# Optimization experiments

Measured on AMD Instinct MI355X. Metric: run time of the kernel, lower is better.

Reference implementation:

```python
import jax, jax.numpy as jnp
import numpy as np

DIM, H, DH = 3072, 24, 128
MLP = int(DIM * 4.0)
EPS = 1e-6


def setup_inputs() -> dict:
    key = jax.random.key(0)
    ks = jax.random.split(key, 8)
    B, L = 2, 4096
    s = 0.02
    return {
        "hidden_states": jax.random.normal(ks[0], (B, L, DIM), jnp.float32),
        "temb": jax.random.normal(ks[1], (B, DIM), jnp.float32),
        "rope": jax.random.normal(ks[2], (L, DH // 2, 4), jnp.float32),
        "w_lin": jax.random.normal(ks[3], (DIM, 3 * DIM), jnp.float32) * s,
        "b_lin": jnp.zeros((3 * DIM,), jnp.float32),
        "w1": jax.random.normal(ks[4], (DIM, 3 * DIM + MLP), jnp.float32) * s,
        "b1": jnp.zeros((3 * DIM + MLP,), jnp.float32),
        "w2": jax.random.normal(ks[5], (DIM + MLP, DIM), jnp.float32) * s,
        "b2": jnp.zeros((DIM,), jnp.float32),
        "q_scale": jnp.ones((DH,), jnp.float32),
        "k_scale": jnp.ones((DH,), jnp.float32),
    }


def _rms(x, scale):
    return x * jax.lax.rsqrt(jnp.mean(x * x, axis=-1, keepdims=True) + EPS) * scale


def _rope(x, fr):
    # x: [B,H,L,DH]; fr: [L, DH//2, 2, 2]
    B, Hn, L, D = x.shape
    x_ = x.reshape(B, Hn, L, D // 2, 1, 2)
    out = fr[..., 0] * x_[..., 0] + fr[..., 1] * x_[..., 1]  # [B,H,L,D//2,2]
    return out.reshape(B, Hn, L, D)


def reference(hidden_states, temb, rope, w_lin, b_lin, w1, b1, w2, b2, q_scale, k_scale):
    B, L, _ = hidden_states.shape
    residual = hidden_states
    # AdaLayerNormZeroSingle
    emb = jax.nn.silu(temb) @ w_lin + b_lin  # [B, 3*DIM]
    shift, scale, gate = jnp.split(emb[:, None, :], 3, axis=-1)
    mu = jnp.mean(hidden_states, axis=-1, keepdims=True)
    var = jnp.mean(jnp.square(hidden_states - mu), axis=-1, keepdims=True)
    x = (hidden_states - mu) * jax.lax.rsqrt(var + EPS)
    x = x * (1 + scale) + shift
    # fused QKV + MLP projection
    proj = x @ w1 + b1
    qkv, mlp = proj[..., : 3 * DIM], proj[..., 3 * DIM :]
    qkv = qkv.reshape(B, L, 3, H, DH).transpose(2, 0, 3, 1, 4)  # [3,B,H,L,DH]
    q, k, v = qkv[0], qkv[1], qkv[2]
    q = _rms(q, q_scale)
    k = _rms(k, k_scale)
    fr = rope.reshape(L, DH // 2, 2, 2)
    q = _rope(q, fr)
    k = _rope(k, fr)
    # heads are MERGED before attention (faithful to source)
    q = q.transpose(0, 2, 1, 3).reshape(B, L, H * DH)
    k = k.transpose(0, 2, 1, 3).reshape(B, L, H * DH)
    v = v.transpose(0, 2, 1, 3).reshape(B, L, H * DH)
    attn = jax.nn.softmax(jnp.einsum("bqd,bkd->bqk", q, k) * (DH ** -0.5), axis=-1)
    attn_out = jnp.einsum("bqk,bkd->bqd", attn, v)
    h = jnp.concatenate([attn_out, jax.nn.gelu(mlp)], axis=-1) @ w2 + b2
    return residual + gate * h
```

## Files before the change

kernel.cpp:

```cpp
#include <hip/hip_runtime.h>
#include <hip/hip_fp16.h>

typedef _Float16 half_t;
typedef __attribute__((ext_vector_type(8))) _Float16 f16x8;
typedef __attribute__((ext_vector_type(4))) float f32x4;

#define DIM   3072
#define NH    24
#define DH    128
#define MLP_D 12288
#define LSEQ  4096
#define BATCH 2
#define NROWS 8192
#define N1    21504
#define QKV_N 9216
#define CAT_N 15360

__device__ __forceinline__ void gload16(const void* g, void* l) {
  __builtin_amdgcn_global_load_lds((const __attribute__((address_space(1))) void*)g,
                                   (__attribute__((address_space(3))) void*)l, 16, 0, 0);
}

__device__ __forceinline__ float gelu_tanh(float x) {
  float u = 0.7978845608028654f * (x + 0.044715f * x * x * x);
  float t = 1.f - 2.f / (__expf(2.f * u) + 1.f);
  return 0.5f * x * (1.f + t);
}

struct EpiParams {
  const float* bias;
  float* outF; int ldoF;
  half_t* o1; int ldo1;
  half_t* o2; int ldo2;
  const float* resid;
  const float* gate;
  float scale;
};

template<int EPI>
__global__ __launch_bounds__(512, 2) void gemm256(
    const half_t* __restrict__ A, int lda,
    const half_t* __restrict__ B, int ldb,
    int nbx, int nby, int nsplit, int K, EpiParams ep)
{
  __shared__ __align__(16) char lds[131072];
  const int t = threadIdx.x, lane = t & 63, wid = t >> 6;

  const int nwg = nbx * nby;
  const int wg = blockIdx.x;
  const int id = (wg & 7) * (nwg >> 3) + (wg >> 3);
  const int panel = 8 * nbx;
  const int bm = (id / panel) * 8 + (id % 8);
  const int bn = (id % panel) / 8;
  const int brow = bm * 256, bcol = bn * 256;
  const int wr = wid >> 2, wc = wid & 3;

  f32x4 acc[8][4];
#pragma unroll
  for (int m = 0; m < 8; ++m)
#pragma unroll
    for (int n = 0; n < 4; ++n) acc[m][n] = (f32x4){0.f, 0.f, 0.f, 0.f};

  const int scol = (((lane & 3) ^ ((lane >> 3) & 3)) * 8);
  const half_t* pA = A + (size_t)(brow + wid * 32 + (lane >> 2)) * lda + scol;
  const half_t* pB = B + (size_t)(bcol + wid * 32 + (lane >> 2)) * ldb + scol;
  const int wrow = wid * 2048;
  const int NT = K >> 5;

  const int pc = (((lane >> 4) ^ ((lane >> 1) & 3)) << 4);
  const int arow = (wr * 128 + (lane & 15)) * 64 + pc;
  const int brow_o = 16384 + (wc * 64 + (lane & 15)) * 64 + pc;

  f16x8 af[4], af2[4], bfA[4], bfB[4];

#define STAGE(tk) {                                                         \
    char* sb = lds + (((tk) & 3) << 15);                                    \
    const half_t* ga = pA + (size_t)(tk) * 32;                              \
    const half_t* gb = pB + (size_t)(tk) * 32;                              \
    gload16(ga, sb + wrow);                                                 \
    gload16(ga + (size_t)16 * lda, sb + wrow + 1024);                       \
    gload16(gb, sb + 16384 + wrow);                                         \
    gload16(gb + (size_t)16 * ldb, sb + 16384 + wrow + 1024); }

#define MFMAC(base, AF, BF)                                                 \
    __builtin_amdgcn_s_setprio(1);                                          \
    _Pragma("unroll")                                                       \
    for (int mi = 0; mi < 4; ++mi)                                          \
      _Pragma("unroll")                                                     \
      for (int nj = 0; nj < 4; ++nj)                                        \
        acc[(base) + mi][nj] = __builtin_amdgcn_mfma_f32_16x16x32_f16(      \
            AF[mi], BF[nj], acc[(base) + mi][nj], 0, 0, 0);                 \
    __builtin_amdgcn_s_setprio(0);

#define BODY(tt, BFC, BFN) {                                                \
    char* cb = lds + (((tt) & 3) << 15);                                    \
    af2[0] = *(const f16x8*)(cb + arow + 4096);                             \
    af2[1] = *(const f16x8*)(cb + arow + 5120);                             \
    af2[2] = *(const f16x8*)(cb + arow + 6144);                             \
    af2[3] = *(const f16x8*)(cb + arow + 7168);                             \
    MFMAC(0, af, BFC)                                                       \
    if ((tt) + 3 < NT) STAGE((tt) + 3);                                     \
    __builtin_amdgcn_sched_barrier(0);                                      \
    if ((tt) + 3 < NT)      asm volatile("s_waitcnt vmcnt(8)" ::: "memory");\
    else if ((tt) + 2 < NT) asm volatile("s_waitcnt vmcnt(4)" ::: "memory");\
    else                    asm volatile("s_waitcnt vmcnt(0)" ::: "memory");\
    __builtin_amdgcn_s_barrier();                                           \
    __builtin_amdgcn_sched_barrier(0);                                      \
    if ((tt) + 1 < NT) {                                                    \
      char* fb = lds + ((((tt) + 1) & 3) << 15);                            \
      af[0] = *(const f16x8*)(fb + arow);                                   \
      af[1] = *(const f16x8*)(fb + arow + 1024);                            \
      af[2] = *(const f16x8*)(fb + arow + 2048);                            \
      af[3] = *(const f16x8*)(fb + arow + 3072);                            \
      BFN[0] = *(const f16x8*)(fb + brow_o);                                \
      BFN[1] = *(const f16x8*)(fb + brow_o + 1024);                         \
      BFN[2] = *(const f16x8*)(fb + brow_o + 2048);                         \
      BFN[3] = *(const f16x8*)(fb + brow_o + 3072);                         \
    }                                                                       \
    MFMAC(4, af2, BFC)                                                      \
  }

  STAGE(0); STAGE(1); STAGE(2);
  asm volatile("s_waitcnt vmcnt(8)" ::: "memory");
  __builtin_amdgcn_s_barrier();
  __builtin_amdgcn_sched_barrier(0);
  af[0] = *(const f16x8*)(lds + arow);
  af[1] = *(const f16x8*)(lds + arow + 1024);
  af[2] = *(const f16x8*)(lds + arow + 2048);
  af[3] = *(const f16x8*)(lds + arow + 3072);
  bfA[0] = *(const f16x8*)(lds + brow_o);
  bfA[1] = *(const f16x8*)(lds + brow_o + 1024);
  bfA[2] = *(const f16x8*)(lds + brow_o + 2048);
  bfA[3] = *(const f16x8*)(lds + brow_o + 3072);

  for (int tt = 0; tt < NT; tt += 2) {
    BODY(tt, bfA, bfB)
    BODY(tt + 1, bfB, bfA)
  }
#undef STAGE
#undef MFMAC
#undef BODY

  const int laneR = lane & 15;
  const int colb = bcol + wc * 64;
  const int rowb = brow + wr * 128 + (lane >> 4) * 4;
#pragma unroll
  for (int mi = 0; mi < 8; ++mi) {
#pragma unroll
    for (int nj = 0; nj < 4; ++nj) {
      int col = colb + nj * 16 + laneR;
#pragma unroll
      for (int j = 0; j < 4; ++j) {
        int row = rowb + mi * 16 + j;
        float v = acc[mi][nj][j];
        if (EPI == 0) {
          v += ep.bias[col];
          if (col < nsplit) {
            ep.o1[(size_t)row * ep.ldo1 + col] = (half_t)v;
          } else {
            ep.o2[(size_t)row * ep.ldo2 + DIM + (col - nsplit)] = (half_t)gelu_tanh(v);
          }
        } else if (EPI == 1) {
          ep.outF[(size_t)row * ep.ldoF + col] = v * ep.scale;
        } else if (EPI == 2) {
          ep.o2[(size_t)row * ep.ldo2 + col] = (half_t)v;
        } else {
          v += ep.bias[col];
          int b = row >> 12;
          float g = ep.gate[(size_t)b * QKV_N + col];
          float r = ep.resid[(size_t)row * DIM + col];
          ep.outF[(size_t)row * ep.ldoF + col] = r + g * v;
        }
      }
    }
  }
}

__global__ __launch_bounds__(256) void k_emb(
    const float* __restrict__ temb, const float* __restrict__ w_lin,
    const float* __restrict__ b_lin, float* __restrict__ emb)
{
  __shared__ float s[DIM];
  int b = blockIdx.y;
  int col = blockIdx.x * 256 + threadIdx.x;
  const float* tr = temb + (size_t)b * DIM;
  for (int k = threadIdx.x; k < DIM; k += 256) {
    float x = tr[k];
    s[k] = x / (1.f + __expf(-x));
  }
  __syncthreads();
  float acc = b_lin[col];
  for (int k = 0; k < DIM; k += 4) {
    acc += s[k] * w_lin[(size_t)k * QKV_N + col]
         + s[k + 1] * w_lin[(size_t)(k + 1) * QKV_N + col]
         + s[k + 2] * w_lin[(size_t)(k + 2) * QKV_N + col]
         + s[k + 3] * w_lin[(size_t)(k + 3) * QKV_N + col];
  }
  emb[(size_t)b * QKV_N + col] = acc;
}

__global__ __launch_bounds__(256) void k_lnmod(
    const float* __restrict__ hs, const float* __restrict__ emb,
    half_t* __restrict__ xmod)
{
  int row = blockIdx.x;
  int b = row >> 12;
  const float* x = hs + (size_t)row * DIM;
  int t = threadIdx.x;
  float s = 0.f, s2 = 0.f;
  float4 v[3];
#pragma unroll
  for (int i = 0; i < 3; ++i) {
    v[i] = ((const float4*)x)[t + 256 * i];
    s  += v[i].x + v[i].y + v[i].z + v[i].w;
    s2 += v[i].x * v[i].x + v[i].y * v[i].y + v[i].z * v[i].z + v[i].w * v[i].w;
  }
  for (int o = 32; o; o >>= 1) { s += __shfl_xor(s, o); s2 += __shfl_xor(s2, o); }
  __shared__ float rs[4], rs2[4];
  int lane = t & 63, w = t >> 6;
  if (lane == 0) { rs[w] = s; rs2[w] = s2; }
  __syncthreads();
  s = rs[0] + rs[1] + rs[2] + rs[3];
  s2 = rs2[0] + rs2[1] + rs2[2] + rs2[3];
  float mu = s * (1.f / DIM);
  float var = s2 * (1.f / DIM) - mu * mu;
  float rstd = rsqrtf(var + 1e-6f);
  const float* shift = emb + (size_t)b * QKV_N;
  const float* scale = shift + DIM;
#pragma unroll
  for (int i = 0; i < 3; ++i) {
    int g = t + 256 * i;
    float4 sc = ((const float4*)scale)[g];
    float4 sh = ((const float4*)shift)[g];
    half_t ob[4];
    float vv[4] = {v[i].x, v[i].y, v[i].z, v[i].w};
    float scv[4] = {sc.x, sc.y, sc.z, sc.w};
    float shv[4] = {sh.x, sh.y, sh.z, sh.w};
#pragma unroll
    for (int j = 0; j < 4; ++j) {
      float xn = (vv[j] - mu) * rstd;
      ob[j] = (half_t)(xn * (1.f + scv[j]) + shv[j]);
    }
    *(uint2*)&xmod[(size_t)row * DIM + g * 4] = *(uint2*)ob;
  }
}

__global__ __launch_bounds__(256) void k_transpose_cvt(
    const float* __restrict__ in, half_t* __restrict__ out, int R, int C)
{
  __shared__ float s[64][65];
  int c0 = blockIdx.x * 64, r0 = blockIdx.y * 64;
  int tx = threadIdx.x & 63, ty = threadIdx.x >> 6;
#pragma unroll
  for (int j = 0; j < 16; ++j) {
    int r = ty + j * 4;
    s[r][tx] = in[(size_t)(r0 + r) * C + c0 + tx];
  }
  __syncthreads();
#pragma unroll
  for (int j = 0; j < 16; ++j) {
    int c = ty + j * 4;
    out[(size_t)(c0 + c) * R + r0 + tx] = (half_t)s[tx][c];
  }
}

__global__ __launch_bounds__(256) void k_qk_rmsrope(
    half_t* __restrict__ qkv, const float* __restrict__ rope,
    const float* __restrict__ q_scale, const float* __restrict__ k_scale)
{
  int w = blockIdx.x * 4 + (threadIdx.x >> 6);
  int lane = threadIdx.x & 63;
  int qk = w & 1;
  int hr = w >> 1;
  int h = hr % 24;
  int bl = hr / 24;
  size_t base = (size_t)bl * QKV_N + qk * DIM + h * DH;
  float x0 = (float)qkv[base + lane * 2];
  float x1 = (float)qkv[base + lane * 2 + 1];
  float ss = x0 * x0 + x1 * x1;
  for (int o = 32; o; o >>= 1) ss += __shfl_xor(ss, o);
  float r = rsqrtf(ss * (1.f / DH) + 1e-6f);
  const float* sc = qk ? k_scale : q_scale;
  float xs0 = x0 * r * sc[lane * 2];
  float xs1 = x1 * r * sc[lane * 2 + 1];
  int l = bl & (LSEQ - 1);
  float4 fr = ((const float4*)rope)[(size_t)l * 64 + lane];
  qkv[base + lane * 2]     = (half_t)(fr.x * xs0 + fr.y * xs1);
  qkv[base + lane * 2 + 1] = (half_t)(fr.z * xs0 + fr.w * xs1);
}

__global__ __launch_bounds__(256) void k_vT(
    const half_t* __restrict__ qkv, half_t* __restrict__ vT)
{
  __shared__ half_t s[64][65];
  int b = blockIdx.z;
  int l0 = blockIdx.x * 64, d0 = blockIdx.y * 64;
  int tx = threadIdx.x & 63, ty = threadIdx.x >> 6;
#pragma unroll
  for (int j = 0; j < 16; ++j) {
    int l = ty + j * 4;
    s[l][tx] = qkv[(size_t)(b * LSEQ + l0 + l) * QKV_N + 2 * DIM + d0 + tx];
  }
  __syncthreads();
#pragma unroll
  for (int j = 0; j < 16; ++j) {
    int d = ty + j * 4;
    vT[((size_t)b * DIM + d0 + d) * LSEQ + l0 + tx] = s[tx][d];
  }
}

__global__ __launch_bounds__(256) void k_softmax(
    const float* __restrict__ S, half_t* __restrict__ P)
{
  int row = blockIdx.x;
  const float* srow = S + (size_t)row * LSEQ;
  int t = threadIdx.x;
  float4 v[4];
  float mx = -1e30f;
#pragma unroll
  for (int i = 0; i < 4; ++i) {
    v[i] = ((const float4*)srow)[t + 256 * i];
    mx = fmaxf(mx, fmaxf(fmaxf(v[i].x, v[i].y), fmaxf(v[i].z, v[i].w)));
  }
  for (int o = 32; o; o >>= 1) mx = fmaxf(mx, __shfl_xor(mx, o));
  __shared__ float rmx[4], rsum[4];
  int lane = t & 63, w = t >> 6;
  if (lane == 0) rmx[w] = mx;
  __syncthreads();
  mx = fmaxf(fmaxf(rmx[0], rmx[1]), fmaxf(rmx[2], rmx[3]));
  float s = 0.f;
#pragma unroll
  for (int i = 0; i < 4; ++i) {
    v[i].x = __expf(v[i].x - mx); v[i].y = __expf(v[i].y - mx);
    v[i].z = __expf(v[i].z - mx); v[i].w = __expf(v[i].w - mx);
    s += v[i].x + v[i].y + v[i].z + v[i].w;
  }
  for (int o = 32; o; o >>= 1) s += __shfl_xor(s, o);
  if (lane == 0) rsum[w] = s;
  __syncthreads();
  s = rsum[0] + rsum[1] + rsum[2] + rsum[3];
  float inv = 1.f / s;
#pragma unroll
  for (int i = 0; i < 4; ++i) {
    half_t ob[4] = {
      (half_t)(v[i].x * inv), (half_t)(v[i].y * inv),
      (half_t)(v[i].z * inv), (half_t)(v[i].w * inv)};
    *(uint2*)&P[(size_t)row * LSEQ + (t + 256 * i) * 4] = *(uint2*)ob;
  }
}

extern "C" void kernel_launch(void* const* d_in, const int* in_sizes, int n_in,
                              void* d_out, int out_size, void* d_ws, size_t ws_size,
                              hipStream_t stream) {
  const float* hs      = (const float*)d_in[0];
  const float* temb    = (const float*)d_in[1];
  const float* rope    = (const float*)d_in[2];
  const float* w_lin   = (const float*)d_in[3];
  const float* b_lin   = (const float*)d_in[4];
  const float* w1      = (const float*)d_in[5];
  const float* b1      = (const float*)d_in[6];
  const float* w2      = (const float*)d_in[7];
  const float* b2      = (const float*)d_in[8];
  const float* q_scale = (const float*)d_in[9];
  const float* k_scale = (const float*)d_in[10];
  float* out = (float*)d_out;

  char* ws = (char*)d_ws;
  size_t off = 0;
  auto alloc = [&](size_t bytes) { char* p = ws + off; off += (bytes + 255) & ~(size_t)255; return p; };
  float*  emb    = (float*) alloc((size_t)BATCH * QKV_N * 4);
  half_t* xmod   = (half_t*)alloc((size_t)NROWS * DIM * 2);
  half_t* w1T    = (half_t*)alloc((size_t)N1 * DIM * 2);
  half_t* w2T    = (half_t*)alloc((size_t)DIM * CAT_N * 2);
  half_t* qkv    = (half_t*)alloc((size_t)NROWS * QKV_N * 2);
  half_t* concat = (half_t*)alloc((size_t)NROWS * CAT_N * 2);
  half_t* vT     = (half_t*)alloc((size_t)BATCH * DIM * LSEQ * 2);
  float*  Sbuf   = (float*) alloc((size_t)LSEQ * LSEQ * 4);
  half_t* Pbuf   = (half_t*)alloc((size_t)LSEQ * LSEQ * 2);
  (void)ws_size; (void)n_in; (void)in_sizes; (void)out_size;

  k_emb<<<dim3(QKV_N / 256, BATCH), 256, 0, stream>>>(temb, w_lin, b_lin, emb);
  k_transpose_cvt<<<dim3(N1 / 64, DIM / 64), 256, 0, stream>>>(w1, w1T, DIM, N1);
  k_transpose_cvt<<<dim3(DIM / 64, CAT_N / 64), 256, 0, stream>>>(w2, w2T, CAT_N, DIM);
  k_lnmod<<<NROWS, 256, 0, stream>>>(hs, emb, xmod);

  EpiParams ep1 = {b1, nullptr, 0, qkv, QKV_N, concat, CAT_N, nullptr, nullptr, 0.f};
  gemm256<0><<<(N1 / 256) * (NROWS / 256), 512, 0, stream>>>(
      xmod, DIM, w1T, DIM, N1 / 256, NROWS / 256, QKV_N, DIM, ep1);

  k_qk_rmsrope<<<(NROWS * NH * 2) / 4, 256, 0, stream>>>(qkv, rope, q_scale, k_scale);
  k_vT<<<dim3(LSEQ / 64, DIM / 64, BATCH), 256, 0, stream>>>(qkv, vT);

  for (int b = 0; b < BATCH; ++b) {
    const half_t* qb = qkv + (size_t)b * LSEQ * QKV_N;
    EpiParams epS = {nullptr, Sbuf, LSEQ, nullptr, 0, nullptr, 0, nullptr, nullptr, 0.08838834764831845f};
    gemm256<1><<<(LSEQ / 256) * (LSEQ / 256), 512, 0, stream>>>(
        qb, QKV_N, qb + DIM, QKV_N, LSEQ / 256, LSEQ / 256, 0, DIM, epS);
    k_softmax<<<LSEQ, 256, 0, stream>>>(Sbuf, Pbuf);
    EpiParams epPV = {nullptr, nullptr, 0, nullptr, 0,
                      concat + (size_t)b * LSEQ * CAT_N, CAT_N, nullptr, nullptr, 0.f};
    gemm256<2><<<(DIM / 256) * (LSEQ / 256), 512, 0, stream>>>(
        Pbuf, LSEQ, vT + (size_t)b * DIM * LSEQ, LSEQ, DIM / 256, LSEQ / 256, 0, LSEQ, epPV);
  }

  EpiParams ep2 = {b2, out, DIM, nullptr, 0, nullptr, 0, hs, emb + 2 * DIM, 0.f};
  gemm256<3><<<(DIM / 256) * (NROWS / 256), 512, 0, stream>>>(
      concat, CAT_N, w2T, CAT_N, DIM / 256, NROWS / 256, 0, CAT_N, ep2);
}
```

Measured before the change: 2.858 ms.

## Load B fragments directly from global into registers, halving LDS use

```diff
diff --git a/kernel.cpp b/kernel.cpp
--- a/kernel.cpp
+++ b/kernel.cpp
@@ -43,7 +43,7 @@
     const half_t* __restrict__ B, int ldb,
     int nbx, int nby, int nsplit, int K, EpiParams ep)
 {
-  __shared__ __align__(16) char lds[131072];
+  __shared__ __align__(16) char lds[65536];
   const int t = threadIdx.x, lane = t & 63, wid = t >> 6;
 
   const int nwg = nbx * nby;
@@ -63,82 +63,70 @@
 
   const int scol = (((lane & 3) ^ ((lane >> 3) & 3)) * 8);
   const half_t* pA = A + (size_t)(brow + wid * 32 + (lane >> 2)) * lda + scol;
-  const half_t* pB = B + (size_t)(bcol + wid * 32 + (lane >> 2)) * ldb + scol;
-  const int wrow = wid * 2048;
   const int NT = K >> 5;
 
   const int pc = (((lane >> 4) ^ ((lane >> 1) & 3)) << 4);
   const int arow = (wr * 128 + (lane & 15)) * 64 + pc;
-  const int brow_o = 16384 + (wc * 64 + (lane & 15)) * 64 + pc;
-
-  f16x8 af[4], af2[4], bfA[4], bfB[4];
-
-#define STAGE(tk) {                                                         \
-    char* sb = lds + (((tk) & 3) << 15);                                    \
+
+  const half_t* pB0 = B + (size_t)(bcol + wc * 64 +  0 + (lane & 15)) * ldb + (lane >> 4) * 8;
+  const half_t* pB1 = B + (size_t)(bcol + wc * 64 + 16 + (lane & 15)) * ldb + (lane >> 4) * 8;
+  const half_t* pB2 = B + (size_t)(bcol + wc * 64 + 32 + (lane & 15)) * ldb + (lane >> 4) * 8;
+  const half_t* pB3 = B + (size_t)(bcol + wc * 64 + 48 + (lane & 15)) * ldb + (lane >> 4) * 8;
+
+  f16x8 bfA[4], bfB[4];
+
+#define STAGE_A(tk) {                                                       \
+    char* sb = lds + (((tk) & 3) << 14);                                    \
     const half_t* ga = pA + (size_t)(tk) * 32;                              \
-    const half_t* gb = pB + (size_t)(tk) * 32;                              \
-    gload16(ga, sb + wrow);                                                 \
-    gload16(ga + (size_t)16 * lda, sb + wrow + 1024);                       \
-    gload16(gb, sb + 16384 + wrow);                                         \
-    gload16(gb + (size_t)16 * ldb, sb + 16384 + wrow + 1024); }
-
-#define MFMAC(base, AF, BF)                                                 \
+    gload16(ga, sb + wid * 2048);                                           \
+    gload16(ga + (size_t)16 * lda, sb + wid * 2048 + 1024); }
+
+#define BODY(tt, BFC, BFN) {                                                \
+    char* cb = lds + (((tt) & 3) << 14);                                    \
+    f16x8 af[8];                                                            \
+    af[0] = *(const f16x8*)(cb + arow);                                     \
+    af[1] = *(const f16x8*)(cb + arow + 1024);                              \
+    af[2] = *(const f16x8*)(cb + arow + 2048);                              \
+    af[3] = *(const f16x8*)(cb + arow + 3072);                              \
+    af[4] = *(const f16x8*)(cb + arow + 4096);                              \
+    af[5] = *(const f16x8*)(cb + arow + 5120);                              \
+    af[6] = *(const f16x8*)(cb + arow + 6144);                              \
+    af[7] = *(const f16x8*)(cb + arow + 7168);                              \
+    if ((tt) + 1 < NT) {                                                    \
+      BFN[0] = *(const f16x8*)(pB0 + (size_t)((tt) + 1) * 32);              \
+      BFN[1] = *(const f16x8*)(pB1 + (size_t)((tt) + 1) * 32);              \
+      BFN[2] = *(const f16x8*)(pB2 + (size_t)((tt) + 1) * 32);              \
+      BFN[3] = *(const f16x8*)(pB3 + (size_t)((tt) + 1) * 32);              \
+    }                                                                       \
+    if ((tt) + 3 < NT) STAGE_A((tt) + 3)                                    \
     __builtin_amdgcn_s_setprio(1);                                          \
     _Pragma("unroll")                                                       \
-    for (int mi = 0; mi < 4; ++mi)                                          \
+    for (int mi = 0; mi < 8; ++mi)                                          \
       _Pragma("unroll")                                                     \
       for (int nj = 0; nj < 4; ++nj)                                        \
-        acc[(base) + mi][nj] = __builtin_amdgcn_mfma_f32_16x16x32_f16(      \
-            AF[mi], BF[nj], acc[(base) + mi][nj], 0, 0, 0);                 \
-    __builtin_amdgcn_s_setprio(0);
-
-#define BODY(tt, BFC, BFN) {                                                \
-    char* cb = lds + (((tt) & 3) << 15);                                    \
-    af2[0] = *(const f16x8*)(cb + arow + 4096);                             \
-    af2[1] = *(const f16x8*)(cb + arow + 5120);                             \
-    af2[2] = *(const f16x8*)(cb + arow + 6144);                             \
-    af2[3] = *(const f16x8*)(cb + arow + 7168);                             \
-    MFMAC(0, af, BFC)                                                       \
-    if ((tt) + 3 < NT) STAGE((tt) + 3);                                     \
+        acc[mi][nj] = __builtin_amdgcn_mfma_f32_16x16x32_f16(               \
+            af[mi], BFC[nj], acc[mi][nj], 0, 0, 0);                         \
+    __builtin_amdgcn_s_setprio(0);                                          \
     __builtin_amdgcn_sched_barrier(0);                                      \
-    if ((tt) + 3 < NT)      asm volatile("s_waitcnt vmcnt(8)" ::: "memory");\
-    else if ((tt) + 2 < NT) asm volatile("s_waitcnt vmcnt(4)" ::: "memory");\
-    else                    asm volatile("s_waitcnt vmcnt(0)" ::: "memory");\
+    if ((tt) + 3 < NT) asm volatile("s_waitcnt vmcnt(8)" ::: "memory");     \
+    else               asm volatile("s_waitcnt vmcnt(0)" ::: "memory");     \
     __builtin_amdgcn_s_barrier();                                           \
-    __builtin_amdgcn_sched_barrier(0);                                      \
-    if ((tt) + 1 < NT) {                                                    \
-      char* fb = lds + ((((tt) + 1) & 3) << 15);                            \
-      af[0] = *(const f16x8*)(fb + arow);                                   \
-      af[1] = *(const f16x8*)(fb + arow + 1024);                            \
-      af[2] = *(const f16x8*)(fb + arow + 2048);                            \
-      af[3] = *(const f16x8*)(fb + arow + 3072);                            \
-      BFN[0] = *(const f16x8*)(fb + brow_o);                                \
-      BFN[1] = *(const f16x8*)(fb + brow_o + 1024);                         \
-      BFN[2] = *(const f16x8*)(fb + brow_o + 2048);                         \
-      BFN[3] = *(const f16x8*)(fb + brow_o + 3072);                         \
-    }                                                                       \
-    MFMAC(4, af2, BFC)                                                      \
-  }
-
-  STAGE(0); STAGE(1); STAGE(2);
-  asm volatile("s_waitcnt vmcnt(8)" ::: "memory");
+    asm volatile("" ::: "memory"); }
+
+  STAGE_A(0) STAGE_A(1) STAGE_A(2)
+  bfA[0] = *(const f16x8*)(pB0);
+  bfA[1] = *(const f16x8*)(pB1);
+  bfA[2] = *(const f16x8*)(pB2);
+  bfA[3] = *(const f16x8*)(pB3);
+  asm volatile("s_waitcnt vmcnt(0)" ::: "memory");
   __builtin_amdgcn_s_barrier();
-  __builtin_amdgcn_sched_barrier(0);
-  af[0] = *(const f16x8*)(lds + arow);
-  af[1] = *(const f16x8*)(lds + arow + 1024);
-  af[2] = *(const f16x8*)(lds + arow + 2048);
-  af[3] = *(const f16x8*)(lds + arow + 3072);
-  bfA[0] = *(const f16x8*)(lds + brow_o);
-  bfA[1] = *(const f16x8*)(lds + brow_o + 1024);
-  bfA[2] = *(const f16x8*)(lds + brow_o + 2048);
-  bfA[3] = *(const f16x8*)(lds + brow_o + 3072);
+  asm volatile("" ::: "memory");
 
   for (int tt = 0; tt < NT; tt += 2) {
     BODY(tt, bfA, bfB)
     BODY(tt + 1, bfB, bfA)
   }
-#undef STAGE
-#undef MFMAC
+#undef STAGE_A
 #undef BODY
 
   const int laneR = lane & 15;
```

Result: slower. 4.355 ms (+52.4%).
